# Performance work log

Hardware: AMD Instinct MI355X
Metric: run time of the kernel (lower is better)

Reference implementation:

```python
import jax, jax.numpy as jnp
import numpy as np

EPS = 0.01  # the module uses 1/sqrt(||x||^2 + 0.01) for cosine normalization


def setup_inputs() -> dict:
    key = jax.random.key(0)
    k1, k2, k3, k4, k5, k6 = jax.random.split(key, 6)
    B, L, L1, D = 512, 256, 256, 128
    sequence = jax.random.randint(k1, (B, L), 0, 10000, dtype=jnp.int32)
    last_sequence = jax.random.randint(k2, (B, L), 0, 2, dtype=jnp.int32)
    sequence_1 = jax.random.randint(k3, (B, L1), 0, 10000, dtype=jnp.int32)
    hist_1 = jax.random.normal(k4, (B, L, D), dtype=jnp.float32)
    hist_2 = jax.random.normal(k5, (B, L1, D), dtype=jnp.float32)
    W = jax.random.normal(k6, (D, D), dtype=jnp.float32) * (1.0 / np.sqrt(D))
    return {"sequence": sequence, "last_sequence": last_sequence,
            "sequence_1": sequence_1, "hist_1": hist_1, "hist_2": hist_2, "W": W}


def reference(sequence, last_sequence, sequence_1, hist_1, hist_2, W):
    # Masks: nonzero ids -> 1.0 (cast to bool then float in the original)
    m = (sequence != 0).astype(jnp.float32)        # [B, L]   key mask for self-attn
    m1 = (sequence_1 != 0).astype(jnp.float32)     # [B, L1]  key mask for cross-attn
    last = last_sequence.astype(jnp.float32)       # [B, L]   last-position indicator

    # --- self cosine-similarity attention over hist_1 ---
    # cos[b,i,j] = <hist_1[b,i], hist_1[b,j]> / (sqrt(||h_i||^2+eps) * sqrt(||h_j||^2+eps))
    dots = jnp.einsum('bid,bjd->bij', hist_1, hist_1)            # [B, L, L]
    inv = jax.lax.rsqrt(jnp.sum(hist_1 * hist_1, axis=-1) + EPS)  # [B, L]
    cos = dots * inv[:, :, None] * inv[:, None, :]
    # softmax-style weighting: exp(cos) masked over keys j (unnormalized exp, per original)
    w = jnp.exp(cos) * m[:, None, :]                             # [B, L, L]
    wsum = jnp.sum(w, axis=-1)                                   # [B, L]
    h_self = jnp.einsum('bij,bjd->bid', w, hist_1) / wsum[..., None]  # [B, L, D]

    # residual add, mask by query validity, then pool at the 'last' position
    h_all_add = (h_self + hist_1) * m[..., None]                 # [B, L, D]
    h_last = jnp.sum(h_all_add * last[..., None], axis=1)        # [B, D]

    # --- cross cosine-similarity attention: h_last attends over hist_2 ---
    dots2 = jnp.einsum('bkd,bd->bk', hist_2, h_last)             # [B, L1]
    inv2k = jax.lax.rsqrt(jnp.sum(hist_2 * hist_2, axis=-1) + EPS)  # [B, L1]
    inv2q = jax.lax.rsqrt(jnp.sum(h_last * h_last, axis=-1) + EPS)  # [B]
    cos2 = dots2 * inv2k * inv2q[:, None]
    w2 = jnp.exp(cos2) * m1                                      # [B, L1]
    h = jnp.einsum('bk,bkd->bd', w2, hist_2) / jnp.sum(w2, axis=-1, keepdims=True)

    out = jax.nn.relu(h @ W)                                     # [B, D]
    return out.reshape(-1, 1, W.shape[0])                        # [B, 1, hidden_num]
```

## Files before the change

kernel.cpp:

```cpp
#include <hip/hip_runtime.h>


using u16 = unsigned short;
using u32 = unsigned int;
typedef __attribute__((ext_vector_type(8))) short bf16x8;
typedef __attribute__((ext_vector_type(4))) float f32x4;
typedef __attribute__((ext_vector_type(4))) u32 u32x4;

#define KST 136
#define KBSZ 4352

__device__ __forceinline__ u16 f2bf(float f) {
  union { float f; u32 i; } v; v.f = f;
  u32 r = v.i + 0x7FFFu + ((v.i >> 16) & 1u);
  return (u16)(r >> 16);
}
__device__ __forceinline__ bf16x8 as_bf(u32x4 x) {
  union { u32x4 u; bf16x8 b; } c; c.u = x; return c.b;
}
__device__ __forceinline__ u32x4 packpair(float4 a, float4 c) {
  u32x4 v;
  v.x = (u32)f2bf(a.x) | ((u32)f2bf(a.y) << 16);
  v.y = (u32)f2bf(a.z) | ((u32)f2bf(a.w) << 16);
  v.z = (u32)f2bf(c.x) | ((u32)f2bf(c.y) << 16);
  v.w = (u32)f2bf(c.z) | ((u32)f2bf(c.w) << 16);
  return v;
}
__device__ __forceinline__ u32x4 pack_bf8(const float* p, float& ss) {
  const float4 a = *(const float4*)p;
  const float4 c = *(const float4*)(p + 4);
  ss += a.x*a.x + a.y*a.y + a.z*a.z + a.w*a.w
      + c.x*c.x + c.y*c.y + c.z*c.z + c.w*c.w;
  return packpair(a, c);
}

__device__ __forceinline__ void stage_k(u32x4 v, float ss, u16* kb,
                                        float* invt, int wv, int q, int m16) {
  const int row = wv * 4 + q;
  *(u32x4*)&kb[row * KST + m16 * 8] = v;
  ss += __shfl_xor(ss, 1); ss += __shfl_xor(ss, 2);
  ss += __shfl_xor(ss, 4); ss += __shfl_xor(ss, 8);
  if (m16 == 0) invt[row] = rsqrtf(ss + 0.01f);
}

__launch_bounds__(1024, 4)
__global__ void itd_fused(const int* __restrict__ seq,
                          const int* __restrict__ lastseq,
                          const int* __restrict__ seq1,
                          const float* __restrict__ h1g,
                          const float* __restrict__ h2g,
                          const float* __restrict__ wg,
                          float* __restrict__ outg) {
  __shared__ unsigned long long SBIG[4224];
  __shared__ float MK[256], LM[256], CJ[256], HLacc[128], HH[128];
  __shared__ float INVT[2][32], WS2[64], SC[2];

  u16* const Kb    = (u16*)SBIG;
  float* const PSC = (float*)SBIG;

  const int b    = blockIdx.x;
  const int t    = threadIdx.x;
  const int lane = t & 63;
  const int wv   = t >> 6;
  const int q    = lane >> 4;
  const int m16  = lane & 15;

  const float* h1b = h1g + (size_t)b * 32768;

  if (t < 256) {
    float m = (seq[b * 256 + t] != 0) ? 1.f : 0.f;
    MK[t] = m;
    LM[t] = m * (float)lastseq[b * 256 + t];
    CJ[t] = 0.f;
  }

  const int i0 = wv * 16;
  u32x4 av[4];
  float invi[4];
  {
    float ss = 0.f;
    #pragma unroll
    for (int s = 0; s < 4; ++s)
      av[s] = pack_bf8(&h1b[(i0 + m16) * 128 + s * 32 + q * 8], ss);
    ss += __shfl_xor(ss, 16);
    ss += __shfl_xor(ss, 32);
    const float invrow = rsqrtf(ss + 0.01f);
    #pragma unroll
    for (int r = 0; r < 4; ++r) invi[r] = __shfl(invrow, q * 4 + r);
  }

  const int srow = wv * 4 + q;
  const int scol = m16 * 8;
  if (t < 512) {
    const float4 a0 = *(const float4*)&h1b[srow * 128 + scol];
    const float4 c0 = *(const float4*)&h1b[srow * 128 + scol + 4];
    float ss = a0.x*a0.x + a0.y*a0.y + a0.z*a0.z + a0.w*a0.w
             + c0.x*c0.x + c0.y*c0.y + c0.z*c0.z + c0.w*c0.w;
    stage_k(packpair(a0, c0), ss, Kb, INVT[0], wv, q, m16);
  }
  __syncthreads();

  const f32x4 fz = {0.f, 0.f, 0.f, 0.f};
  float wpart[4] = {0.f, 0.f, 0.f, 0.f};
  float coef[4];

  for (int jt = 0; jt < 16; ++jt) {
    const int cur  = jt & 1;
    const int tile = jt & 7;
    float4 pfa, pfb;
    if (t < 512 && jt < 15) {
      const float* np = &h1b[((jt + 1) & 7) * 4096 + srow * 128 + scol];
      pfa = *(const float4*)np;
      pfb = *(const float4*)(np + 4);
    }

    f32x4 Sa = fz, Sb = fz;
    const u16* kb = Kb + cur * KBSZ;
    #pragma unroll
    for (int s = 0; s < 4; ++s) {
      bf16x8 ba = *(const bf16x8*)&kb[m16 * KST + s * 32 + q * 8];
      bf16x8 bb = *(const bf16x8*)&kb[(16 + m16) * KST + s * 32 + q * 8];
      bf16x8 af = as_bf(av[s]);
      Sa = __builtin_amdgcn_mfma_f32_16x16x32_bf16(af, ba, Sa, 0, 0, 0);
      Sb = __builtin_amdgcn_mfma_f32_16x16x32_bf16(af, bb, Sb, 0, 0, 0);
    }
    const float invja = INVT[cur][m16];
    const float invjb = INVT[cur][16 + m16];
    if (jt < 8) {
      const float mja = MK[tile * 32 + m16];
      const float mjb = MK[tile * 32 + 16 + m16];
      #pragma unroll
      for (int r = 0; r < 4; ++r) {
        wpart[r] += __expf(Sa[r] * (invi[r] * invja)) * mja
                  + __expf(Sb[r] * (invi[r] * invjb)) * mjb;
      }
      if (jt == 7) {
        #pragma unroll
        for (int r = 0; r < 4; ++r) {
          float s = wpart[r];
          s += __shfl_xor(s, 1); s += __shfl_xor(s, 2);
          s += __shfl_xor(s, 4); s += __shfl_xor(s, 8);
          coef[r] = LM[i0 + q * 4 + r] / s;
        }
      }
    } else {
      float ca = 0.f, cb = 0.f;
      #pragma unroll
      for (int r = 0; r < 4; ++r) {
        ca += coef[r] * __expf(Sa[r] * (invi[r] * invja));
        cb += coef[r] * __expf(Sb[r] * (invi[r] * invjb));
      }
      ca += __shfl_xor(ca, 16); ca += __shfl_xor(ca, 32);
      cb += __shfl_xor(cb, 16); cb += __shfl_xor(cb, 32);
      if (q == 0) {
        atomicAdd(&CJ[tile * 32 + m16], ca);
        atomicAdd(&CJ[tile * 32 + 16 + m16], cb);
      }
    }

    if (t < 512 && jt < 15) {
      float ss = pfa.x*pfa.x + pfa.y*pfa.y + pfa.z*pfa.z + pfa.w*pfa.w
               + pfb.x*pfb.x + pfb.y*pfb.y + pfb.z*pfb.z + pfb.w*pfb.w;
      stage_k(packpair(pfa, pfb), ss, Kb + (cur ^ 1) * KBSZ,
              INVT[cur ^ 1], wv, q, m16);
    }
    __syncthreads();
  }

  if (t < 256) CJ[t] = MK[t] * CJ[t] + LM[t];
  __syncthreads();

  {
    const int g = t >> 7, dd = t & 127;
    float p = 0.f;
    #pragma unroll 8
    for (int n = 0; n < 32; ++n)
      p += CJ[g * 32 + n] * h1b[(g * 32 + n) * 128 + dd];
    PSC[g * 132 + dd] = p;
  }
  __syncthreads();
  if (t < 128) {
    float s = 0.f;
    #pragma unroll
    for (int g = 0; g < 8; ++g) s += PSC[g * 132 + t];
    HLacc[t] = s;
  }
  __syncthreads();

  if (t < 64) {
    float s = HLacc[t] * HLacc[t] + HLacc[t + 64] * HLacc[t + 64];
    s += __shfl_xor(s, 1); s += __shfl_xor(s, 2); s += __shfl_xor(s, 4);
    s += __shfl_xor(s, 8); s += __shfl_xor(s, 16); s += __shfl_xor(s, 32);
    if (t == 0) SC[0] = rsqrtf(s + 0.01f);
  }
  if (t < 256) MK[t] = (seq1[b * 256 + t] != 0) ? 1.f : 0.f;
  __syncthreads();

  const float* h2b = h2g + (size_t)b * 32768;
  if (t < 512) {
    const int row8 = lane >> 3;
    const int sub  = lane & 7;
    const int slot = wv * 8 + row8;
    const float invq = SC[0];
    f32x4 acc4[4];
    #pragma unroll
    for (int c = 0; c < 4; ++c) acc4[c] = {0.f, 0.f, 0.f, 0.f};
    float ws2 = 0.f;
    const float* hl = &HLacc[sub * 4];
    #pragma unroll
    for (int kt = 0; kt < 4; ++kt) {
      const int k = kt * 64 + slot;
      const float* rowp = h2b + k * 128 + sub * 4;
      const float4 v0 = *(const float4*)(rowp);
      const float4 v1 = *(const float4*)(rowp + 32);
      const float4 v2 = *(const float4*)(rowp + 64);
      const float4 v3 = *(const float4*)(rowp + 96);
      float dot = v0.x*hl[0]  + v0.y*hl[1]  + v0.z*hl[2]  + v0.w*hl[3]
                + v1.x*hl[32] + v1.y*hl[33] + v1.z*hl[34] + v1.w*hl[35]
                + v2.x*hl[64] + v2.y*hl[65] + v2.z*hl[66] + v2.w*hl[67]
                + v3.x*hl[96] + v3.y*hl[97] + v3.z*hl[98] + v3.w*hl[99];
      float ss  = v0.x*v0.x + v0.y*v0.y + v0.z*v0.z + v0.w*v0.w
                + v1.x*v1.x + v1.y*v1.y + v1.z*v1.z + v1.w*v1.w
                + v2.x*v2.x + v2.y*v2.y + v2.z*v2.z + v2.w*v2.w
                + v3.x*v3.x + v3.y*v3.y + v3.z*v3.z + v3.w*v3.w;
      dot += __shfl_xor(dot, 1); dot += __shfl_xor(dot, 2); dot += __shfl_xor(dot, 4);
      ss  += __shfl_xor(ss, 1);  ss  += __shfl_xor(ss, 2);  ss  += __shfl_xor(ss, 4);
      const float w2 = __expf(dot * rsqrtf(ss + 0.01f) * invq) * MK[k];
      ws2 += w2;
      acc4[0][0] += w2*v0.x; acc4[0][1] += w2*v0.y; acc4[0][2] += w2*v0.z; acc4[0][3] += w2*v0.w;
      acc4[1][0] += w2*v1.x; acc4[1][1] += w2*v1.y; acc4[1][2] += w2*v1.z; acc4[1][3] += w2*v1.w;
      acc4[2][0] += w2*v2.x; acc4[2][1] += w2*v2.y; acc4[2][2] += w2*v2.z; acc4[2][3] += w2*v2.w;
      acc4[3][0] += w2*v3.x; acc4[3][1] += w2*v3.y; acc4[3][2] += w2*v3.z; acc4[3][3] += w2*v3.w;
    }
    #pragma unroll
    for (int c = 0; c < 4; ++c)
      *(f32x4*)&PSC[slot * 132 + c * 32 + sub * 4] = acc4[c];
    if (sub == 0) WS2[slot] = ws2;
  }
  __syncthreads();

  float hsum = 0.f;
  if (t < 128) {
    #pragma unroll
    for (int n = 0; n < 64; ++n) hsum += PSC[n * 132 + t];
  }
  if (t < 64) {
    float s = WS2[t];
    s += __shfl_xor(s, 1); s += __shfl_xor(s, 2); s += __shfl_xor(s, 4);
    s += __shfl_xor(s, 8); s += __shfl_xor(s, 16); s += __shfl_xor(s, 32);
    if (t == 0) SC[1] = s;
  }
  __syncthreads();
  if (t < 128) HH[t] = hsum / SC[1];
  __syncthreads();

  if (t < 128) {
    float o = 0.f;
    #pragma unroll 8
    for (int d = 0; d < 128; ++d)
      o += HH[d] * wg[d * 128 + t];
    outg[(size_t)b * 128 + t] = fmaxf(o, 0.f);
  }
}

extern "C" void kernel_launch(void* const* d_in, const int* in_sizes, int n_in,
                              void* d_out, int out_size, void* d_ws, size_t ws_size,
                              hipStream_t stream) {
  (void)in_sizes; (void)n_in; (void)d_ws; (void)ws_size; (void)out_size;
  const int*   seq     = (const int*)d_in[0];
  const int*   lastseq = (const int*)d_in[1];
  const int*   seq1    = (const int*)d_in[2];
  const float* h1      = (const float*)d_in[3];
  const float* h2      = (const float*)d_in[4];
  const float* w       = (const float*)d_in[5];
  float* out           = (float*)d_out;
  itd_fused<<<dim3(512), dim3(1024), 0, stream>>>(seq, lastseq, seq1, h1, h2, w, out);
}
```

Measured before the change: 209.1 us.

## Halve block size, stage 128-row K tiles with XOR swizzle, two row tiles per wave

Blocks now have 512 threads instead of 1024, and each wave computes two 16-row query tiles, so every K fragment read from LDS feeds four MFMAs instead of two. K is staged in 128-row halves, with a per-128-byte XOR swizzle replacing padding, across four phases: two for the row sums and two for the coefficients. This replaces the per-32-row double-buffered prefetch. The key mask and inverse norm are folded into a scale and a -1e38 bias fused into one fma before exp, which removes the multiply by the mask. In exchange, global loads no longer overlap with MFMA work, since K is loaded synchronously at the start of each phase, and each thread holds more registers.

```diff
diff --git a/kernel.cpp b/kernel.cpp
--- a/kernel.cpp
+++ b/kernel.cpp
@@ -6,9 +6,6 @@
 typedef __attribute__((ext_vector_type(8))) short bf16x8;
 typedef __attribute__((ext_vector_type(4))) float f32x4;
 typedef __attribute__((ext_vector_type(4))) u32 u32x4;
-
-#define KST 136
-#define KBSZ 4352
 
 __device__ __forceinline__ u16 f2bf(float f) {
   union { float f; u32 i; } v; v.f = f;
@@ -34,16 +31,7 @@
   return packpair(a, c);
 }
 
-__device__ __forceinline__ void stage_k(u32x4 v, float ss, u16* kb,
-                                        float* invt, int wv, int q, int m16) {
-  const int row = wv * 4 + q;
-  *(u32x4*)&kb[row * KST + m16 * 8] = v;
-  ss += __shfl_xor(ss, 1); ss += __shfl_xor(ss, 2);
-  ss += __shfl_xor(ss, 4); ss += __shfl_xor(ss, 8);
-  if (m16 == 0) invt[row] = rsqrtf(ss + 0.01f);
-}
-
-__launch_bounds__(1024, 4)
+__launch_bounds__(512)
 __global__ void itd_fused(const int* __restrict__ seq,
                           const int* __restrict__ lastseq,
                           const int* __restrict__ seq1,
@@ -52,10 +40,11 @@
                           const float* __restrict__ wg,
                           float* __restrict__ outg) {
   __shared__ unsigned long long SBIG[4224];
-  __shared__ float MK[256], LM[256], CJ[256], HLacc[128], HH[128];
-  __shared__ float INVT[2][32], WS2[64], SC[2];
-
-  u16* const Kb    = (u16*)SBIG;
+  __shared__ float MK[256], LM[256], CJ[256];
+  __shared__ float SCL[128], SBS[128];
+  __shared__ float HLacc[128], HH[128], WS2[64], SC[2];
+
+  u16* const   KS  = (u16*)SBIG;
   float* const PSC = (float*)SBIG;
 
   const int b    = blockIdx.x;
@@ -74,98 +63,115 @@
     CJ[t] = 0.f;
   }
 
-  const int i0 = wv * 16;
-  u32x4 av[4];
-  float invi[4];
-  {
+  u32x4 av[2][4];
+  float invi[2][4];
+  #pragma unroll
+  for (int rt = 0; rt < 2; ++rt) {
+    const int i0q = wv * 32 + rt * 16;
     float ss = 0.f;
     #pragma unroll
     for (int s = 0; s < 4; ++s)
-      av[s] = pack_bf8(&h1b[(i0 + m16) * 128 + s * 32 + q * 8], ss);
+      av[rt][s] = pack_bf8(&h1b[(i0q + m16) * 128 + s * 32 + q * 8], ss);
     ss += __shfl_xor(ss, 16);
     ss += __shfl_xor(ss, 32);
     const float invrow = rsqrtf(ss + 0.01f);
     #pragma unroll
-    for (int r = 0; r < 4; ++r) invi[r] = __shfl(invrow, q * 4 + r);
-  }
-
-  const int srow = wv * 4 + q;
-  const int scol = m16 * 8;
-  if (t < 512) {
-    const float4 a0 = *(const float4*)&h1b[srow * 128 + scol];
-    const float4 c0 = *(const float4*)&h1b[srow * 128 + scol + 4];
-    float ss = a0.x*a0.x + a0.y*a0.y + a0.z*a0.z + a0.w*a0.w
-             + c0.x*c0.x + c0.y*c0.y + c0.z*c0.z + c0.w*c0.w;
-    stage_k(packpair(a0, c0), ss, Kb, INVT[0], wv, q, m16);
-  }
-  __syncthreads();
+    for (int r = 0; r < 4; ++r) invi[rt][r] = __shfl(invrow, q * 4 + r);
+  }
+
+  const int sr  = t >> 2;
+  const int scs = (t & 3) * 32;
+  const int xsw = (m16 & 7) << 4;
 
   const f32x4 fz = {0.f, 0.f, 0.f, 0.f};
-  float wpart[4] = {0.f, 0.f, 0.f, 0.f};
-  float coef[4];
-
-  for (int jt = 0; jt < 16; ++jt) {
-    const int cur  = jt & 1;
-    const int tile = jt & 7;
-    float4 pfa, pfb;
-    if (t < 512 && jt < 15) {
-      const float* np = &h1b[((jt + 1) & 7) * 4096 + srow * 128 + scol];
-      pfa = *(const float4*)np;
-      pfb = *(const float4*)(np + 4);
-    }
-
-    f32x4 Sa = fz, Sb = fz;
-    const u16* kb = Kb + cur * KBSZ;
-    #pragma unroll
-    for (int s = 0; s < 4; ++s) {
-      bf16x8 ba = *(const bf16x8*)&kb[m16 * KST + s * 32 + q * 8];
-      bf16x8 bb = *(const bf16x8*)&kb[(16 + m16) * KST + s * 32 + q * 8];
-      bf16x8 af = as_bf(av[s]);
-      Sa = __builtin_amdgcn_mfma_f32_16x16x32_bf16(af, ba, Sa, 0, 0, 0);
-      Sb = __builtin_amdgcn_mfma_f32_16x16x32_bf16(af, bb, Sb, 0, 0, 0);
-    }
-    const float invja = INVT[cur][m16];
-    const float invjb = INVT[cur][16 + m16];
-    if (jt < 8) {
-      const float mja = MK[tile * 32 + m16];
-      const float mjb = MK[tile * 32 + 16 + m16];
+  float wpart[2][4] = {{0.f,0.f,0.f,0.f},{0.f,0.f,0.f,0.f}};
+  float coef[2][4];
+
+  for (int ph = 0; ph < 4; ++ph) {
+    const int h = ph & 1;
+    __syncthreads();
+    {
+      const float* p = h1b + (h * 128 + sr) * 128 + scs;
+      float ss = 0.f;
+      u32x4 w0 = pack_bf8(p, ss);
+      u32x4 w1 = pack_bf8(p + 8, ss);
+      u32x4 w2 = pack_bf8(p + 16, ss);
+      u32x4 w3 = pack_bf8(p + 24, ss);
+      ss += __shfl_xor(ss, 1);
+      ss += __shfl_xor(ss, 2);
+      char* kbB = (char*)KS + sr * 256;
+      const int bb = scs * 2, xr = (sr & 7) << 4;
+      *(u32x4*)(kbB + ((bb)      ^ xr)) = w0;
+      *(u32x4*)(kbB + ((bb + 16) ^ xr)) = w1;
+      *(u32x4*)(kbB + ((bb + 32) ^ xr)) = w2;
+      *(u32x4*)(kbB + ((bb + 48) ^ xr)) = w3;
+      if ((t & 3) == 0) {
+        const float m = MK[h * 128 + sr];
+        const float inv = rsqrtf(ss + 0.01f);
+        SCL[sr] = (m > 0.f) ? inv : 0.f;
+        SBS[sr] = (m > 0.f) ? 0.f : -1e38f;
+      }
+    }
+    __syncthreads();
+
+    for (int tl = 0; tl < 4; ++tl) {
+      f32x4 Sa[2] = {fz, fz}, Sb[2] = {fz, fz};
+      const char* kbB = (const char*)KS;
+      const int rowA = (tl * 32 + m16) * 256;
+      const int rowB = (tl * 32 + 16 + m16) * 256;
       #pragma unroll
-      for (int r = 0; r < 4; ++r) {
-        wpart[r] += __expf(Sa[r] * (invi[r] * invja)) * mja
-                  + __expf(Sb[r] * (invi[r] * invjb)) * mjb;
+      for (int s = 0; s < 4; ++s) {
+        const int co = (s * 64 + q * 16) ^ xsw;
+        const bf16x8 ba = *(const bf16x8*)(kbB + rowA + co);
+        const bf16x8 bb = *(const bf16x8*)(kbB + rowB + co);
+        const bf16x8 a0 = as_bf(av[0][s]);
+        const bf16x8 a1 = as_bf(av[1][s]);
+        Sa[0] = __builtin_amdgcn_mfma_f32_16x16x32_bf16(a0, ba, Sa[0], 0, 0, 0);
+        Sb[0] = __builtin_amdgcn_mfma_f32_16x16x32_bf16(a0, bb, Sb[0], 0, 0, 0);
+        Sa[1] = __builtin_amdgcn_mfma_f32_16x16x32_bf16(a1, ba, Sa[1], 0, 0, 0);
+        Sb[1] = __builtin_amdgcn_mfma_f32_16x16x32_bf16(a1, bb, Sb[1], 0, 0, 0);
       }
-      if (jt == 7) {
+      const float sA = SCL[tl * 32 + m16],      bA = SBS[tl * 32 + m16];
+      const float sB = SCL[tl * 32 + 16 + m16], bB = SBS[tl * 32 + 16 + m16];
+      if (ph < 2) {
+        #pragma unroll
+        for (int rt = 0; rt < 2; ++rt)
+          #pragma unroll
+          for (int r = 0; r < 4; ++r) {
+            wpart[rt][r] += __expf(fmaf(Sa[rt][r] * invi[rt][r], sA, bA))
+                          + __expf(fmaf(Sb[rt][r] * invi[rt][r], sB, bB));
+          }
+      } else {
+        float cA = 0.f, cB = 0.f;
+        #pragma unroll
+        for (int rt = 0; rt < 2; ++rt)
+          #pragma unroll
+          for (int r = 0; r < 4; ++r) {
+            cA += coef[rt][r] * __expf(fmaf(Sa[rt][r] * invi[rt][r], sA, bA));
+            cB += coef[rt][r] * __expf(fmaf(Sb[rt][r] * invi[rt][r], sB, bB));
+          }
+        cA += __shfl_xor(cA, 16); cA += __shfl_xor(cA, 32);
+        cB += __shfl_xor(cB, 16); cB += __shfl_xor(cB, 32);
+        if (q == 0) {
+          atomicAdd(&CJ[h * 128 + tl * 32 + m16], cA);
+          atomicAdd(&CJ[h * 128 + tl * 32 + 16 + m16], cB);
+        }
+      }
+    }
+
+    if (ph == 1) {
+      #pragma unroll
+      for (int rt = 0; rt < 2; ++rt)
         #pragma unroll
         for (int r = 0; r < 4; ++r) {
-          float s = wpart[r];
+          float s = wpart[rt][r];
           s += __shfl_xor(s, 1); s += __shfl_xor(s, 2);
           s += __shfl_xor(s, 4); s += __shfl_xor(s, 8);
-          coef[r] = LM[i0 + q * 4 + r] / s;
+          coef[rt][r] = LM[wv * 32 + rt * 16 + q * 4 + r] / s;
         }
-      }
-    } else {
-      float ca = 0.f, cb = 0.f;
-      #pragma unroll
-      for (int r = 0; r < 4; ++r) {
-        ca += coef[r] * __expf(Sa[r] * (invi[r] * invja));
-        cb += coef[r] * __expf(Sb[r] * (invi[r] * invjb));
-      }
-      ca += __shfl_xor(ca, 16); ca += __shfl_xor(ca, 32);
-      cb += __shfl_xor(cb, 16); cb += __shfl_xor(cb, 32);
-      if (q == 0) {
-        atomicAdd(&CJ[tile * 32 + m16], ca);
-        atomicAdd(&CJ[tile * 32 + 16 + m16], cb);
-      }
-    }
-
-    if (t < 512 && jt < 15) {
-      float ss = pfa.x*pfa.x + pfa.y*pfa.y + pfa.z*pfa.z + pfa.w*pfa.w
-               + pfb.x*pfb.x + pfb.y*pfb.y + pfb.z*pfb.z + pfb.w*pfb.w;
-      stage_k(packpair(pfa, pfb), ss, Kb + (cur ^ 1) * KBSZ,
-              INVT[cur ^ 1], wv, q, m16);
-    }
-    __syncthreads();
-  }
+    }
+  }
+  __syncthreads();
 
   if (t < 256) CJ[t] = MK[t] * CJ[t] + LM[t];
   __syncthreads();
@@ -174,17 +180,13 @@
     const int g = t >> 7, dd = t & 127;
     float p = 0.f;
     #pragma unroll 8
-    for (int n = 0; n < 32; ++n)
-      p += CJ[g * 32 + n] * h1b[(g * 32 + n) * 128 + dd];
+    for (int n = 0; n < 64; ++n)
+      p += CJ[g * 64 + n] * h1b[(g * 64 + n) * 128 + dd];
     PSC[g * 132 + dd] = p;
   }
   __syncthreads();
-  if (t < 128) {
-    float s = 0.f;
-    #pragma unroll
-    for (int g = 0; g < 8; ++g) s += PSC[g * 132 + t];
-    HLacc[t] = s;
-  }
+  if (t < 128)
+    HLacc[t] = PSC[t] + PSC[132 + t] + PSC[264 + t] + PSC[396 + t];
   __syncthreads();
 
   if (t < 64) {
@@ -197,7 +199,7 @@
   __syncthreads();
 
   const float* h2b = h2g + (size_t)b * 32768;
-  if (t < 512) {
+  {
     const int row8 = lane >> 3;
     const int sub  = lane & 7;
     const int slot = wv * 8 + row8;
@@ -274,5 +276,5 @@
   const float* h2      = (const float*)d_in[4];
   const float* w       = (const float*)d_in[5];
   float* out           = (float*)d_out;
-  itd_fused<<<dim3(512), dim3(1024), 0, stream>>>(seq, lastseq, seq1, h1, h2, w, out);
-}
+  itd_fused<<<dim3(512), dim3(512), 0, stream>>>(seq, lastseq, seq1, h1, h2, w, out);
+}
```

Result: faster. 203.8 us (-2.5%).
